# Performance work log

Measured on AMD Instinct MI355X. Metric: run time of the kernel, lower is better.

## Reference

```python
import jax, jax.numpy as jnp
import numpy as np

N = 100000          # nodes
E = 1000000         # edges (before self-loops)
NFEAT = 512
NHID = 32
HEADS = 8
NCLASS = 40
SLOPE = 0.2         # PyG GATConv negative_slope


def gat_conv(x, W, a_src, a_dst, bias, src, dst, heads, out_c, concat):
    """PyG-style GATConv (eval mode, self-loops already appended to src/dst)."""
    n = x.shape[0]
    h = (x @ W).reshape(n, heads, out_c)                      # [N, H, C]
    e_src = jnp.sum(h * a_src, axis=-1)                       # [N, H]
    e_dst = jnp.sum(h * a_dst, axis=-1)                       # [N, H]
    e = jax.nn.leaky_relu(e_src[src] + e_dst[dst], SLOPE)     # [E, H]
    m = jax.ops.segment_max(e, dst, num_segments=n)           # per-dst max
    ex = jnp.exp(e - m[dst])
    den = jax.ops.segment_sum(ex, dst, num_segments=n)        # [N, H]
    alpha = ex / den[dst]                                     # softmax over in-edges
    out = jax.ops.segment_sum(alpha[:, :, None] * h[src], dst, num_segments=n)
    out = out.reshape(n, heads * out_c) if concat else out.mean(axis=1)
    return out + bias


def setup_inputs() -> dict:
    key = jax.random.key(0)
    ks = jax.random.split(key, 10)
    x = jax.random.normal(ks[0], (N, NFEAT), dtype=jnp.float32)
    edge_index = jax.random.randint(ks[1], (2, E), 0, N, dtype=jnp.int64)
    s1 = 1.0 / np.sqrt(NFEAT)
    s2 = 1.0 / np.sqrt(HEADS * NHID)
    return {
        "x": x,
        "edge_index": edge_index,
        "W1": jax.random.normal(ks[2], (NFEAT, HEADS * NHID), dtype=jnp.float32) * s1,
        "a_src1": jax.random.normal(ks[3], (HEADS, NHID), dtype=jnp.float32) * s2,
        "a_dst1": jax.random.normal(ks[4], (HEADS, NHID), dtype=jnp.float32) * s2,
        "b1": jnp.zeros((HEADS * NHID,), dtype=jnp.float32),
        "W2": jax.random.normal(ks[5], (HEADS * NHID, NCLASS), dtype=jnp.float32) * s2,
        "a_src2": jax.random.normal(ks[6], (1, NCLASS), dtype=jnp.float32) * 0.1,
        "a_dst2": jax.random.normal(ks[7], (1, NCLASS), dtype=jnp.float32) * 0.1,
        "b2": jnp.zeros((NCLASS,), dtype=jnp.float32),
    }


def reference(x, edge_index, W1, a_src1, a_dst1, b1, W2, a_src2, a_dst2, b2):
    loop = jnp.arange(N, dtype=edge_index.dtype)
    src = jnp.concatenate([edge_index[0], loop])
    dst = jnp.concatenate([edge_index[1], loop])
    # layer 1: nfeat -> heads*nhid (concat), ELU  (dropout is identity in eval)
    h1 = jax.nn.elu(gat_conv(x, W1, a_src1, a_dst1, b1, src, dst, HEADS, NHID, True))
    # layer 2: heads*nhid -> nclass, single head, concat=False
    logits = gat_conv(h1, W2, a_src2, a_dst2, b2, src, dst, 1, NCLASS, False)
    return jax.nn.log_softmax(logits, axis=1), h1
```

## Files before the change

kernel.cpp:

```cpp
#include <hip/hip_runtime.h>

#define NN 100000
#define EE 1000000
#define NFEAT 512
#define NHID 32
#define HEADS 8
#define F1 256
#define NCLASS 40
#define SLOPE 0.2f
#define NB1 98

typedef __bf16 bf16x8 __attribute__((ext_vector_type(8)));
typedef float f32x4 __attribute__((ext_vector_type(4)));

union BF8 { unsigned short s[8]; bf16x8 v; uint4 u; };

__device__ __forceinline__ float bf2f(unsigned short u) {
    return __uint_as_float(((unsigned)u) << 16);
}
__device__ __forceinline__ unsigned short f2bf(float f) {
    unsigned x = __float_as_uint(f);
    unsigned r = (x + 0x7fffu + ((x >> 16) & 1u)) >> 16;
    return (unsigned short)r;
}
__device__ __forceinline__ float lrelu(float x) { return x > 0.f ? x : SLOPE * x; }

__global__ void detect_i64(const int* __restrict__ ei, int* __restrict__ flag) {
    int i = blockIdx.x * 256 + threadIdx.x;
    if (i < 4096) {
        if (ei[2 * i + 1] != 0) atomicOr(flag, 1);
    }
}
__global__ void canon_edges(const int* __restrict__ ei, const int* __restrict__ flag,
                            int* __restrict__ srcC, int* __restrict__ dstC,
                            int* __restrict__ deg) {
    int e = blockIdx.x * 256 + threadIdx.x;
    if (e >= EE) return;
    int s, d;
    if (*flag) {
        s = ei[e];
        d = ei[EE + e];
    } else {
        int2 a = ((const int2*)ei)[e];
        int2 b = ((const int2*)ei)[EE + e];
        s = a.x;
        d = b.x;
    }
    srcC[e] = s;
    dstC[e] = d;
    atomicAdd(deg + d, 1);
}

__global__ void scan1(const int* __restrict__ deg, int* __restrict__ bsum) {
    __shared__ int s[256];
    int b = blockIdx.x, t = threadIdx.x;
    int base = b * 1024 + t * 4, sum = 0;
    #pragma unroll
    for (int j = 0; j < 4; j++) { int i = base + j; sum += (i < NN) ? deg[i] : 0; }
    s[t] = sum; __syncthreads();
    for (int off = 128; off > 0; off >>= 1) {
        if (t < off) s[t] += s[t + off];
        __syncthreads();
    }
    if (t == 0) bsum[b] = s[0];
}
__global__ void scan2(int* __restrict__ bsum, int* __restrict__ row_ptr) {
    int lane = threadIdx.x;
    int v0 = (lane < NB1) ? bsum[lane] : 0;
    int v1 = (64 + lane < NB1) ? bsum[64 + lane] : 0;
    int s0 = v0;
    #pragma unroll
    for (int off = 1; off < 64; off <<= 1) {
        int t = __shfl_up(s0, off);
        if (lane >= off) s0 += t;
    }
    int tot0 = __shfl(s0, 63);
    int s1 = v1;
    #pragma unroll
    for (int off = 1; off < 64; off <<= 1) {
        int t = __shfl_up(s1, off);
        if (lane >= off) s1 += t;
    }
    s1 += tot0;
    if (lane < NB1) bsum[lane] = s0 - v0;
    if (64 + lane < NB1) bsum[64 + lane] = s1 - v1;
    if (lane == 0) row_ptr[NN] = EE;
}
__global__ void scan3(const int* __restrict__ deg, const int* __restrict__ bsum,
                      int* __restrict__ row_ptr, int* __restrict__ pos) {
    __shared__ int ts[256];
    int b = blockIdx.x, t = threadIdx.x;
    int base = b * 1024 + t * 4;
    int v[4], sum = 0;
    #pragma unroll
    for (int j = 0; j < 4; j++) { int i = base + j; v[j] = (i < NN) ? deg[i] : 0; sum += v[j]; }
    ts[t] = sum; __syncthreads();
    for (int off = 1; off < 256; off <<= 1) {
        int add = (t >= off) ? ts[t - off] : 0;
        __syncthreads();
        ts[t] += add;
        __syncthreads();
    }
    int prefix = bsum[b] + ts[t] - sum;
    #pragma unroll
    for (int j = 0; j < 4; j++) {
        int i = base + j;
        if (i < NN) { row_ptr[i] = prefix; pos[i] = prefix; prefix += v[j]; }
    }
}
__global__ void fill_csr(const int* __restrict__ srcC, const int* __restrict__ dstC,
                         int* __restrict__ pos, int* __restrict__ eadj) {
    int e = blockIdx.x * 256 + threadIdx.x;
    if (e >= EE) return;
    int idx = atomicAdd(pos + dstC[e], 1);
    eadj[idx] = srcC[e];
}

__global__ void prep_w1(const float* __restrict__ w1, unsigned short* __restrict__ w1tb) {
    int t = blockIdx.x * 256 + threadIdx.x;
    if (t < NFEAT * F1) {
        int k = t / F1, n = t % F1;
        w1tb[n * NFEAT + k] = f2bf(w1[t]);
    }
}

__device__ __forceinline__ void stage_b(const unsigned short* __restrict__ w1tb,
                                        unsigned short* bs, int kk, int tid) {
    #pragma unroll
    for (int j = 0; j < 4; j++) {
        int c = j * 256 + tid;
        int n = c >> 2, part = c & 3;
        const unsigned short* src = w1tb + n * NFEAT + kk * 32 + part * 8;
        unsigned short* dst = bs + c * 8;
        __builtin_amdgcn_global_load_lds(
            (const __attribute__((address_space(1))) unsigned int*)src,
            (__attribute__((address_space(3))) unsigned int*)dst, 16, 0, 0);
    }
}

__global__ __launch_bounds__(256) void gemm1_kernel(
    const float* __restrict__ x, const unsigned short* __restrict__ w1tb,
    const float* __restrict__ a_src, const float* __restrict__ a_dst,
    unsigned short* __restrict__ hb, float* __restrict__ es, float* __restrict__ ed) {
    __shared__ unsigned short Bs[2][256 * 32];
    __shared__ float As_[F1], Ad_[F1];
    int tid = threadIdx.x;
    As_[tid] = a_src[tid];
    Ad_[tid] = a_dst[tid];
    int wave = tid >> 6, lane = tid & 63;
    int quad = lane >> 4, r = lane & 15;
    int mBase = blockIdx.x * 64 + wave * 16;
    long arow = mBase + r; if (arow > NN - 1) arow = NN - 1;
    const float* aptr = x + arow * NFEAT + quad * 8;

    stage_b(w1tb, Bs[0], 0, tid);

    f32x4 acc[16];
    #pragma unroll
    for (int t = 0; t < 16; t++) acc[t] = {0.f, 0.f, 0.f, 0.f};

    for (int kk = 0; kk < 16; kk++) {
        float4 fa0 = *(const float4*)(aptr + kk * 32);
        float4 fa1 = *(const float4*)(aptr + kk * 32 + 4);
        float fa[8] = {fa0.x, fa0.y, fa0.z, fa0.w, fa1.x, fa1.y, fa1.z, fa1.w};
        BF8 ah;
        #pragma unroll
        for (int j = 0; j < 8; j++) ah.s[j] = f2bf(fa[j]);
        __syncthreads();
        if (kk + 1 < 16) stage_b(w1tb, Bs[(kk + 1) & 1], kk + 1, tid);
        const unsigned short* bsc = Bs[kk & 1];
        #pragma unroll
        for (int t = 0; t < 16; t++) {
            BF8 vb;
            vb.u = *(const uint4*)(bsc + (t * 16 + r) * 32 + quad * 8);
            acc[t] = __builtin_amdgcn_mfma_f32_16x16x32_bf16(ah.v, vb.v, acc[t], 0, 0, 0);
        }
    }
    #pragma unroll
    for (int i = 0; i < 4; i++) {
        int m = mBase + quad * 4 + i;
        if (m < NN) {
            unsigned short* hp = hb + (long)m * F1 + r;
            #pragma unroll
            for (int t = 0; t < 16; t++) hp[t * 16] = f2bf(acc[t][i]);
        }
        float pv[16];
        #pragma unroll
        for (int k = 0; k < 16; k++) pv[k] = 0.f;
        #pragma unroll
        for (int t = 0; t < 16; t++) {
            float hv = bf2f(f2bf(acc[t][i]));
            int hd = t >> 1;
            pv[hd]     += hv * As_[t * 16 + r];
            pv[8 + hd] += hv * Ad_[t * 16 + r];
        }
        #pragma unroll
        for (int b = 1; b <= 8; b <<= 1) {
            #pragma unroll
            for (int k = 0; k < 16; k++) pv[k] += __shfl_xor(pv[k], b);
        }
        if (m < NN) {
            float v = pv[0];
            #pragma unroll
            for (int k = 1; k < 16; k++) v = (r == k) ? pv[k] : v;
            int hd = r & 7;
            if (r < 8) es[(long)m * 8 + hd] = v;
            else       ed[(long)m * 8 + hd] = v;
        }
    }
}

__global__ __launch_bounds__(256) void gat1_fused(
    const int* __restrict__ row_ptr, const int* __restrict__ eadj,
    const float* __restrict__ es, const float* __restrict__ ed,
    const unsigned short* __restrict__ hb, const float* __restrict__ b1,
    float* __restrict__ h1o) {
    int wave = threadIdx.x >> 6, lane = threadIdx.x & 63;
    int d = blockIdx.x * 4 + wave;
    if (d >= NN) return;
    int eslot = lane >> 3, hd8 = lane & 7;
    int half = lane >> 5, sub = lane & 31, hh = sub >> 2;
    float edv = ed[d * 8 + hd8];
    int beg = row_ptr[d], end = row_ptr[d + 1];

    float mself = lrelu(es[d * 8 + hd8] + edv);
    float m = mself;
    float den = (eslot == 0) ? 1.f : 0.f;

    float a0, a1, a2, a3, a4, a5, a6, a7;
    if (half == 0) {
        uint4 u = ((const uint4*)(hb + (long)d * F1))[sub];
        a0 = bf2f((unsigned short)(u.x & 0xffffu)); a1 = bf2f((unsigned short)(u.x >> 16));
        a2 = bf2f((unsigned short)(u.y & 0xffffu)); a3 = bf2f((unsigned short)(u.y >> 16));
        a4 = bf2f((unsigned short)(u.z & 0xffffu)); a5 = bf2f((unsigned short)(u.z >> 16));
        a6 = bf2f((unsigned short)(u.w & 0xffffu)); a7 = bf2f((unsigned short)(u.w >> 16));
    } else {
        a0 = a1 = a2 = a3 = a4 = a5 = a6 = a7 = 0.f;
    }

    for (int i = beg; i < end; i += 8) {
        int idx = i + eslot;
        int s = (idx < end) ? eadj[idx] : 0;
        float el = lrelu(es[s * 8 + hd8] + edv);
        if (idx >= end) el = -1e30f;
        float gm = el;
        gm = fmaxf(gm, __shfl_xor(gm, 8));
        gm = fmaxf(gm, __shfl_xor(gm, 16));
        gm = fmaxf(gm, __shfl_xor(gm, 32));
        float mn = fmaxf(m, gm);
        float rsc = __expf(m - mn);
        m = mn;
        den *= rsc;
        float wj = (idx < end) ? __expf(el - m) : 0.f;
        den += wj;
        float ro = __shfl(rsc, hh);
        a0 *= ro; a1 *= ro; a2 *= ro; a3 *= ro;
        a4 *= ro; a5 *= ro; a6 *= ro; a7 *= ro;

        int cnt = min(8, end - i);
        #pragma unroll
        for (int jj = 0; jj < 4; jj++) {
            int e = jj * 2 + half;
            float w = __shfl(wj, e * 8 + hh);
            int sj = __shfl(s, e * 8);
            if (e < cnt) {
                uint4 u = ((const uint4*)(hb + (long)sj * F1))[sub];
                a0 += w * bf2f((unsigned short)(u.x & 0xffffu));
                a1 += w * bf2f((unsigned short)(u.x >> 16));
                a2 += w * bf2f((unsigned short)(u.y & 0xffffu));
                a3 += w * bf2f((unsigned short)(u.y >> 16));
                a4 += w * bf2f((unsigned short)(u.z & 0xffffu));
                a5 += w * bf2f((unsigned short)(u.z >> 16));
                a6 += w * bf2f((unsigned short)(u.w & 0xffffu));
                a7 += w * bf2f((unsigned short)(u.w >> 16));
            }
        }
    }
    den += __shfl_xor(den, 8);
    den += __shfl_xor(den, 16);
    den += __shfl_xor(den, 32);
    float deno = __shfl(den, hh);

    a0 += __shfl_xor(a0, 32); a1 += __shfl_xor(a1, 32);
    a2 += __shfl_xor(a2, 32); a3 += __shfl_xor(a3, 32);
    a4 += __shfl_xor(a4, 32); a5 += __shfl_xor(a5, 32);
    a6 += __shfl_xor(a6, 32); a7 += __shfl_xor(a7, 32);

    if (half == 0) {
        float inv = 1.f / deno;
        float4 blo = ((const float4*)b1)[sub * 2];
        float4 bhi = ((const float4*)b1)[sub * 2 + 1];
        float r0 = a0 * inv + blo.x, r1 = a1 * inv + blo.y;
        float r2 = a2 * inv + blo.z, r3 = a3 * inv + blo.w;
        float r4 = a4 * inv + bhi.x, r5 = a5 * inv + bhi.y;
        float r6 = a6 * inv + bhi.z, r7 = a7 * inv + bhi.w;
        r0 = r0 > 0.f ? r0 : expm1f(r0); r1 = r1 > 0.f ? r1 : expm1f(r1);
        r2 = r2 > 0.f ? r2 : expm1f(r2); r3 = r3 > 0.f ? r3 : expm1f(r3);
        r4 = r4 > 0.f ? r4 : expm1f(r4); r5 = r5 > 0.f ? r5 : expm1f(r5);
        r6 = r6 > 0.f ? r6 : expm1f(r6); r7 = r7 > 0.f ? r7 : expm1f(r7);
        float4 o0 = {r0, r1, r2, r3}, o1 = {r4, r5, r6, r7};
        ((float4*)(h1o + (long)d * F1))[sub * 2] = o0;
        ((float4*)(h1o + (long)d * F1))[sub * 2 + 1] = o1;
    }
}

__global__ __launch_bounds__(256) void gemm2_kernel(const float* __restrict__ h1,
                                                    const float* __restrict__ w2,
                                                    float* __restrict__ h2) {
    __shared__ float4 Ws[F1 * 10];
    for (int i = threadIdx.x; i < F1 * 10; i += 256) Ws[i] = ((const float4*)w2)[i];
    __syncthreads();
    long t = (long)blockIdx.x * 256 + threadIdx.x;
    if (t >= (long)NN * 10) return;
    int n = (int)(t / 10);
    int j = (int)(t - (long)n * 10);
    const float4* hp = (const float4*)(h1 + (long)n * F1);
    float4 a = {0.f, 0.f, 0.f, 0.f};
    #pragma unroll 8
    for (int k4 = 0; k4 < 64; k4++) {
        float4 hv = hp[k4];
        float4 w0 = Ws[(k4 * 4 + 0) * 10 + j];
        float4 w1v = Ws[(k4 * 4 + 1) * 10 + j];
        float4 w2v = Ws[(k4 * 4 + 2) * 10 + j];
        float4 w3v = Ws[(k4 * 4 + 3) * 10 + j];
        a.x += hv.x * w0.x + hv.y * w1v.x + hv.z * w2v.x + hv.w * w3v.x;
        a.y += hv.x * w0.y + hv.y * w1v.y + hv.z * w2v.y + hv.w * w3v.y;
        a.z += hv.x * w0.z + hv.y * w1v.z + hv.z * w2v.z + hv.w * w3v.z;
        a.w += hv.x * w0.w + hv.y * w1v.w + hv.z * w2v.w + hv.w * w3v.w;
    }
    ((float4*)(h2 + (long)n * NCLASS))[j] = a;
}

__global__ void escore2_kernel(const float* __restrict__ h2,
                               const float* __restrict__ a_src2,
                               const float* __restrict__ a_dst2,
                               float* __restrict__ e2s, float* __restrict__ e2d) {
    __shared__ float As[NCLASS], Ad[NCLASS];
    if (threadIdx.x < NCLASS) {
        As[threadIdx.x] = a_src2[threadIdx.x];
        Ad[threadIdx.x] = a_dst2[threadIdx.x];
    }
    __syncthreads();
    int n = blockIdx.x * 256 + threadIdx.x;
    if (n >= NN) return;
    const float* hp = h2 + (long)n * NCLASS;
    float s = 0.f, d = 0.f;
    #pragma unroll
    for (int c = 0; c < NCLASS; c++) {
        float v = hp[c];
        s += v * As[c];
        d += v * Ad[c];
    }
    e2s[n] = s; e2d[n] = d;
}

__global__ __launch_bounds__(256) void gat2_logsm(
    const int* __restrict__ row_ptr, const int* __restrict__ eadj,
    const float* __restrict__ e2s, const float* __restrict__ e2d,
    const float* __restrict__ h2, const float* __restrict__ b2,
    float* __restrict__ out0) {
    int wave = threadIdx.x >> 6, lane = threadIdx.x & 63;
    int d = blockIdx.x * 4 + wave;
    if (d >= NN) return;
    int eslot = lane >> 3, c8 = lane & 7;
    float edv = e2d[d];
    int beg = row_ptr[d], end = row_ptr[d + 1];

    float mself = lrelu(e2s[d] + edv);
    float m = mself;
    float den = (eslot == 0) ? 1.f : 0.f;
    float acc[5];
    {
        const float* hp = h2 + (long)d * NCLASS + c8 * 5;
        #pragma unroll
        for (int k = 0; k < 5; k++) acc[k] = (eslot == 0) ? hp[k] : 0.f;
    }

    for (int i = beg; i < end; i += 8) {
        int idx = i + eslot;
        int s = (idx < end) ? eadj[idx] : 0;
        float el = lrelu(e2s[s] + edv);
        if (idx >= end) el = -1e30f;
        float gm = el;
        gm = fmaxf(gm, __shfl_xor(gm, 8));
        gm = fmaxf(gm, __shfl_xor(gm, 16));
        gm = fmaxf(gm, __shfl_xor(gm, 32));
        float mn = fmaxf(m, gm);
        float rsc = __expf(m - mn);
        m = mn;
        den *= rsc;
        #pragma unroll
        for (int k = 0; k < 5; k++) acc[k] *= rsc;
        float wj = (idx < end) ? __expf(el - m) : 0.f;
        den += wj;
        if (idx < end) {
            const float* hp = h2 + (long)s * NCLASS + c8 * 5;
            #pragma unroll
            for (int k = 0; k < 5; k++) acc[k] += wj * hp[k];
        }
    }
    #pragma unroll
    for (int off = 8; off <= 32; off <<= 1) {
        den += __shfl_xor(den, off);
        #pragma unroll
        for (int k = 0; k < 5; k++) acc[k] += __shfl_xor(acc[k], off);
    }
    float inv = 1.f / den;
    float v[5];
    float mx = -1e30f;
    #pragma unroll
    for (int k = 0; k < 5; k++) {
        v[k] = acc[k] * inv + b2[c8 * 5 + k];
        mx = fmaxf(mx, v[k]);
    }
    #pragma unroll
    for (int off = 1; off <= 4; off <<= 1) mx = fmaxf(mx, __shfl_xor(mx, off));
    float sm = 0.f;
    #pragma unroll
    for (int k = 0; k < 5; k++) sm += __expf(v[k] - mx);
    #pragma unroll
    for (int off = 1; off <= 4; off <<= 1) sm += __shfl_xor(sm, off);
    float ls = mx + logf(sm);
    if (eslot == 0) {
        float* op = out0 + (long)d * NCLASS + c8 * 5;
        #pragma unroll
        for (int k = 0; k < 5; k++) op[k] = v[k] - ls;
    }
}

extern "C" void kernel_launch(void* const* d_in, const int* in_sizes, int n_in,
                              void* d_out, int out_size, void* d_ws, size_t ws_size,
                              hipStream_t stream) {
    const float* x   = (const float*)d_in[0];
    const int* ei    = (const int*)d_in[1];
    const float* W1  = (const float*)d_in[2];
    const float* as1 = (const float*)d_in[3];
    const float* ad1 = (const float*)d_in[4];
    const float* b1  = (const float*)d_in[5];
    const float* W2  = (const float*)d_in[6];
    const float* as2 = (const float*)d_in[7];
    const float* ad2 = (const float*)d_in[8];
    const float* b2  = (const float*)d_in[9];

    float* out0 = (float*)d_out;
    float* h1o  = out0 + (long)NN * NCLASS;

    unsigned short* hb = (unsigned short*)d_ws;
    unsigned short* w1tb = hb + (long)NN * F1;
    float* es1  = (float*)(w1tb + F1 * NFEAT);
    float* ed1  = es1 + NN * HEADS;
    float* e2s  = ed1 + NN * HEADS;
    float* e2d  = e2s + NN;
    int* srcC   = (int*)(e2d + NN);
    int* dstC   = srcC + EE;
    int* eadj   = dstC + EE;
    int* deg    = eadj + EE;
    int* row_ptr= deg + NN;
    int* pos    = row_ptr + NN + 1;
    int* bsum   = pos + NN;
    int* flag   = bsum + NB1;
    float* h2   = (float*)d_ws;

    hipMemsetAsync(flag, 0, 4, stream);
    hipMemsetAsync(deg, 0, (size_t)NN * 4, stream);

    detect_i64<<<16, 256, 0, stream>>>(ei, flag);
    canon_edges<<<(EE + 255) / 256, 256, 0, stream>>>(ei, flag, srcC, dstC, deg);
    scan1<<<NB1, 256, 0, stream>>>(deg, bsum);
    scan2<<<1, 64, 0, stream>>>(bsum, row_ptr);
    scan3<<<NB1, 256, 0, stream>>>(deg, bsum, row_ptr, pos);
    fill_csr<<<(EE + 255) / 256, 256, 0, stream>>>(srcC, dstC, pos, eadj);

    prep_w1<<<(NFEAT * F1 + 255) / 256, 256, 0, stream>>>(W1, w1tb);
    gemm1_kernel<<<(NN + 63) / 64, 256, 0, stream>>>(x, w1tb, as1, ad1, hb, es1, ed1);
    gat1_fused<<<(NN + 3) / 4, 256, 0, stream>>>(row_ptr, eadj, es1, ed1, hb, b1, h1o);

    gemm2_kernel<<<(int)(((long)NN * 10 + 255) / 256), 256, 0, stream>>>(h1o, W2, h2);
    escore2_kernel<<<(NN + 255) / 256, 256, 0, stream>>>(h2, as2, ad2, e2s, e2d);
    gat2_logsm<<<(NN + 3) / 4, 256, 0, stream>>>(row_ptr, eadj, e2s, e2d, h2, b2, out0);
}
```

Baseline: 711.5 us.

## Prefetch GEMM A tiles, swizzle B LDS layout, prefetch edge indices in aggregation

In the layer-1 GEMM, the next k-slice of x is loaded into registers one iteration early. The barrier and B staging move to the top of the loop so the loads overlap the MFMA work. The B tile in LDS is reordered so each quad's 16-byte reads are contiguous, which should reduce bank conflicts. In both aggregation kernels the next edge source index is loaded one iteration ahead, hiding the dependent gather latency at the cost of extra registers.

```diff
diff --git a/kernel.cpp b/kernel.cpp
--- a/kernel.cpp
+++ b/kernel.cpp
@@ -128,10 +128,13 @@
                                         unsigned short* bs, int kk, int tid) {
     #pragma unroll
     for (int j = 0; j < 4; j++) {
-        int c = j * 256 + tid;
-        int n = c >> 2, part = c & 3;
-        const unsigned short* src = w1tb + n * NFEAT + kk * 32 + part * 8;
-        unsigned short* dst = bs + c * 8;
+        int p = j * 256 + tid;
+        int tq = p >> 6;
+        int qd = (p >> 4) & 3;
+        int rr = p & 15;
+        int n = tq * 16 + rr;
+        const unsigned short* src = w1tb + n * NFEAT + kk * 32 + qd * 8;
+        unsigned short* dst = bs + p * 8;
         __builtin_amdgcn_global_load_lds(
             (const __attribute__((address_space(1))) unsigned int*)src,
             (__attribute__((address_space(3))) unsigned int*)dst, 16, 0, 0);
@@ -154,27 +157,33 @@
     const float* aptr = x + arow * NFEAT + quad * 8;
 
     stage_b(w1tb, Bs[0], 0, tid);
+    float4 fa0 = *(const float4*)(aptr);
+    float4 fa1 = *(const float4*)(aptr + 4);
 
     f32x4 acc[16];
     #pragma unroll
     for (int t = 0; t < 16; t++) acc[t] = {0.f, 0.f, 0.f, 0.f};
 
     for (int kk = 0; kk < 16; kk++) {
-        float4 fa0 = *(const float4*)(aptr + kk * 32);
-        float4 fa1 = *(const float4*)(aptr + kk * 32 + 4);
+        __syncthreads();
+        float4 nf0, nf1;
+        if (kk + 1 < 16) {
+            stage_b(w1tb, Bs[(kk + 1) & 1], kk + 1, tid);
+            nf0 = *(const float4*)(aptr + (kk + 1) * 32);
+            nf1 = *(const float4*)(aptr + (kk + 1) * 32 + 4);
+        }
         float fa[8] = {fa0.x, fa0.y, fa0.z, fa0.w, fa1.x, fa1.y, fa1.z, fa1.w};
         BF8 ah;
         #pragma unroll
         for (int j = 0; j < 8; j++) ah.s[j] = f2bf(fa[j]);
-        __syncthreads();
-        if (kk + 1 < 16) stage_b(w1tb, Bs[(kk + 1) & 1], kk + 1, tid);
         const unsigned short* bsc = Bs[kk & 1];
         #pragma unroll
         for (int t = 0; t < 16; t++) {
             BF8 vb;
-            vb.u = *(const uint4*)(bsc + (t * 16 + r) * 32 + quad * 8);
+            vb.u = *(const uint4*)(bsc + (t * 64 + quad * 16 + r) * 8);
             acc[t] = __builtin_amdgcn_mfma_f32_16x16x32_bf16(ah.v, vb.v, acc[t], 0, 0, 0);
         }
+        if (kk + 1 < 16) { fa0 = nf0; fa1 = nf1; }
     }
     #pragma unroll
     for (int i = 0; i < 4; i++) {
@@ -238,9 +247,14 @@
         a0 = a1 = a2 = a3 = a4 = a5 = a6 = a7 = 0.f;
     }
 
+    int sPre = (beg + eslot < end) ? eadj[beg + eslot] : 0;
     for (int i = beg; i < end; i += 8) {
         int idx = i + eslot;
-        int s = (idx < end) ? eadj[idx] : 0;
+        int s = sPre;
+        if (i + 8 < end) {
+            int nidx = idx + 8;
+            sPre = (nidx < end) ? eadj[nidx] : 0;
+        }
         float el = lrelu(es[s * 8 + hd8] + edv);
         if (idx >= end) el = -1e30f;
         float gm = el;
@@ -376,9 +390,14 @@
         for (int k = 0; k < 5; k++) acc[k] = (eslot == 0) ? hp[k] : 0.f;
     }
 
+    int sPre = (beg + eslot < end) ? eadj[beg + eslot] : 0;
     for (int i = beg; i < end; i += 8) {
         int idx = i + eslot;
-        int s = (idx < end) ? eadj[idx] : 0;
+        int s = sPre;
+        if (i + 8 < end) {
+            int nidx = idx + 8;
+            sPre = (nidx < end) ? eadj[nidx] : 0;
+        }
         float el = lrelu(e2s[s] + edv);
         if (idx >= end) el = -1e30f;
         float gm = el;
```

Result: slower. 740.9 us (+4.1%).
